# Kernel tuning notes

Hardware: AMD Instinct MI355X
Metric: run time of the kernel (lower is better)

The kernel has to match this reference:

```python
import jax, jax.numpy as jnp
import numpy as np

T, D, E, K, F, SF = 4096, 1024, 8, 2, 1024, 1024  # tokens, d_model, experts, top_k, moe_ff, shared_ff


def setup_inputs() -> dict:
    key = jax.random.key(0)
    ks = jax.random.split(key, 10)
    hidden_states = jax.random.normal(ks[0], (T, D), jnp.float32)
    # balanced expert assignment: the fused kernel's get_split_sizes assumes tokens
    # split evenly across experts after permute_tokens, so exactly T*K/E per expert
    flat = jnp.arange(T * K) % E
    flat = jax.random.permutation(ks[1], flat)
    topk_indices = flat.reshape(T, K).astype(jnp.int32)
    w = jax.random.uniform(ks[2], (T, K), jnp.float32)
    topk_weights = w / w.sum(-1, keepdims=True)  # norm_topk_prob
    s = 0.02
    w_gate = jax.random.normal(ks[3], (E, D, F), jnp.float32) * s
    w_up = jax.random.normal(ks[4], (E, D, F), jnp.float32) * s
    w_down = jax.random.normal(ks[5], (E, F, D), jnp.float32) * s
    sw_gate = jax.random.normal(ks[6], (D, SF), jnp.float32) * s
    sw_up = jax.random.normal(ks[7], (D, SF), jnp.float32) * s
    sw_down = jax.random.normal(ks[8], (SF, D), jnp.float32) * s
    shared_gate_w = jax.random.normal(ks[9], (D, 1), jnp.float32) * s
    return dict(hidden_states=hidden_states, topk_weights=topk_weights,
                w_gate=w_gate, w_up=w_up, w_down=w_down,
                sw_gate=sw_gate, sw_up=sw_up, sw_down=sw_down,
                shared_gate_w=shared_gate_w, topk_indices=topk_indices)


def _silu(x):
    return x * jax.nn.sigmoid(x)


def reference(hidden_states, topk_weights, w_gate, w_up, w_down,
              sw_gate, sw_up, sw_down, shared_gate_w, topk_indices):
    t, d = hidden_states.shape
    e = w_gate.shape[0]
    k = topk_indices.shape[1]
    c = (t * k) // e  # tokens per expert (balanced split, as in get_split_sizes)

    # permute_tokens: replicate each token top_k times and sort by expert id
    flat_idx = topk_indices.reshape(-1)                    # [t*k]
    order = jnp.argsort(flat_idx)                          # dispatch permutation
    x_rep = jnp.repeat(hidden_states, k, axis=0)           # [t*k, d]
    xs = x_rep[order].reshape(e, c, d)                     # grouped per-expert

    # per-expert gated MLP (grouped GEMMs)
    h = _silu(jnp.einsum('ecd,edf->ecf', xs, w_gate)) * jnp.einsum('ecd,edf->ecf', xs, w_up)
    y = jnp.einsum('ecf,efd->ecd', h, w_down).reshape(t * k, d)

    # unpermute_tokens + weighted combine over top_k
    y = y[jnp.argsort(order)].reshape(t, k, d)
    out = (y * topk_weights[..., None]).sum(axis=1)        # [t, d]

    # shared expert with sigmoid gate
    s = jnp.einsum('tf,fd->td', _silu(hidden_states @ sw_gate) * (hidden_states @ sw_up), sw_down)
    g = jax.nn.sigmoid(hidden_states @ shared_gate_w)      # [t, 1]
    return (out + g * s).astype(hidden_states.dtype)
```

## Files before the change

### kernel.cpp

```cpp
#include <hip/hip_runtime.h>
#include <hip/hip_bf16.h>
#include <cstdint>
#include <cstddef>

#define TTOK 4096
#define DM   1024
#define NE   8
#define KTOP 2
#define FFD  1024
#define CPER 1024
#define MROWS 12288


typedef __attribute__((ext_vector_type(8))) short frag8;
typedef __attribute__((ext_vector_type(4))) float f32x4;

static __device__ __forceinline__ unsigned short f2bf(float f) {
  unsigned int u = __float_as_uint(f);
  u += 0x7fff + ((u >> 16) & 1);
  return (unsigned short)(u >> 16);
}
static __device__ __forceinline__ float bf2f(unsigned short u) {
  return __uint_as_float((unsigned int)u << 16);
}

static __device__ __forceinline__ void gld_lds16(const unsigned short* g, unsigned short* l) {
  __builtin_amdgcn_global_load_lds(
      (const __attribute__((address_space(1))) unsigned int*)g,
      (__attribute__((address_space(3))) unsigned int*)l,
      16, 0, 0);
}

static __device__ __forceinline__ int lds_slot64(int r, int c) {
  return r * 8 + (c ^ (r & 7));
}

static __device__ __forceinline__ void stage_tile64(const unsigned short* __restrict__ src,
                                                    int row0, int k0,
                                                    unsigned short* lds, int tid) {
#pragma unroll
  for (int it = 0; it < 4; ++it) {
    int seg = it * 256 + tid;
    int r = seg >> 3;
    int cs = (seg & 7) ^ (r & 7);
    gld_lds16(src + (size_t)(row0 + r) * 1024 + k0 + cs * 8, lds + seg * 8);
  }
}

static __device__ __forceinline__ void swizzle_xy(int& x, int& y) {
  int L = blockIdx.y * 8 + blockIdx.x;
  int xcd = L & 7;
  int s = L >> 3;
  y = xcd * 12 + s % 12;
  x = s / 12;
}

static __device__ __forceinline__ void swizzle_xy4(int& x, int& y) {
  int L = blockIdx.y * 4 + blockIdx.x;
  int xcd = L & 7;
  int s = L >> 3;
  y = xcd * 12 + s % 12;
  x = s / 12;
}

__global__ void prep_transw_kernel(
    const float* __restrict__ wg, const float* __restrict__ wu,
    const float* __restrict__ wd, const float* __restrict__ sg,
    const float* __restrict__ su, const float* __restrict__ sd,
    unsigned short* __restrict__ owg, unsigned short* __restrict__ owu,
    unsigned short* __restrict__ owd,
    const float* __restrict__ x, const float* __restrict__ gw,
    const int* __restrict__ idx, const float* __restrict__ tw,
    int* __restrict__ cnt, int* __restrict__ rowsrc, int* __restrict__ inv,
    float* __restrict__ rowscale, unsigned short* __restrict__ xb) {
  int z = blockIdx.z;
  if (z == 27) {
    int bid = blockIdx.y * 4 + blockIdx.x;
    if (bid < 32) {
      int i = bid * 256 + threadIdx.x;
      int e = idx[i];
      int pos = atomicAdd(&cnt[e], 1);
      int j = e * CPER + pos;
      rowsrc[j] = i >> 1;
      rowscale[j] = tw[i];
      inv[i] = j;
      if (i < TTOK) rowsrc[8192 + i] = i;
    }
    int wave = threadIdx.x >> 6;
    int lane = threadIdx.x & 63;
    const float4* wr = (const float4*)gw;
#pragma unroll 2
    for (int s = 0; s < 16; ++s) {
      int row = bid * 64 + wave * 16 + s;
      const float4* xr = (const float4*)(x + (size_t)row * 1024);
      ushort4* ob = (ushort4*)(xb + (size_t)row * 1024);
      float acc = 0.f;
#pragma unroll
      for (int c = 0; c < 4; ++c) {
        int k = lane + 64 * c;
        float4 v = xr[k];
        float4 g = wr[k];
        acc += v.x * g.x + v.y * g.y + v.z * g.z + v.w * g.w;
        ushort4 o;
        o.x = f2bf(v.x); o.y = f2bf(v.y); o.z = f2bf(v.z); o.w = f2bf(v.w);
        ob[k] = o;
      }
#pragma unroll
      for (int off = 32; off; off >>= 1) acc += __shfl_down(acc, off);
      if (lane == 0) rowscale[8192 + row] = 1.f / (1.f + __expf(-acc));
    }
    return;
  }
  const float* src; unsigned short* dst;
  if (z < 8)       { src = wg + (size_t)z * 1048576;        dst = owg + (size_t)z * 1048576; }
  else if (z < 16) { src = wu + (size_t)(z - 8) * 1048576;  dst = owu + (size_t)(z - 8) * 1048576; }
  else if (z < 24) { src = wd + (size_t)(z - 16) * 1048576; dst = owd + (size_t)(z - 16) * 1048576; }
  else if (z == 24){ src = sg; dst = owg + (size_t)8 * 1048576; }
  else if (z == 25){ src = su; dst = owu + (size_t)8 * 1048576; }
  else             { src = sd; dst = owd + (size_t)8 * 1048576; }
  __shared__ float tile[64][65];
  int bx0 = blockIdx.x * 256;
  int by  = blockIdx.y * 64;
  int c4 = threadIdx.x & 15;
  int r0 = threadIdx.x >> 4;
  const float* sbase = src + (size_t)(by + r0) * 1024 + bx0 + c4 * 4;
  float4 v0 = *(const float4*)(sbase + 0);
  float4 v1 = *(const float4*)(sbase + 16384);
  float4 v2 = *(const float4*)(sbase + 32768);
  float4 v3 = *(const float4*)(sbase + 49152);
  float4 w0, w1, w2, w3;
#pragma unroll
  for (int t = 0; t < 4; ++t) {
    int bx = bx0 + t * 64;
    __syncthreads();
    tile[r0     ][c4 * 4 + 0] = v0.x; tile[r0     ][c4 * 4 + 1] = v0.y;
    tile[r0     ][c4 * 4 + 2] = v0.z; tile[r0     ][c4 * 4 + 3] = v0.w;
    tile[r0 + 16][c4 * 4 + 0] = v1.x; tile[r0 + 16][c4 * 4 + 1] = v1.y;
    tile[r0 + 16][c4 * 4 + 2] = v1.z; tile[r0 + 16][c4 * 4 + 3] = v1.w;
    tile[r0 + 32][c4 * 4 + 0] = v2.x; tile[r0 + 32][c4 * 4 + 1] = v2.y;
    tile[r0 + 32][c4 * 4 + 2] = v2.z; tile[r0 + 32][c4 * 4 + 3] = v2.w;
    tile[r0 + 48][c4 * 4 + 0] = v3.x; tile[r0 + 48][c4 * 4 + 1] = v3.y;
    tile[r0 + 48][c4 * 4 + 2] = v3.z; tile[r0 + 48][c4 * 4 + 3] = v3.w;
    if (t < 3) {
      const float* nb = sbase + (t + 1) * 64;
      w0 = *(const float4*)(nb + 0);
      w1 = *(const float4*)(nb + 16384);
      w2 = *(const float4*)(nb + 32768);
      w3 = *(const float4*)(nb + 49152);
    }
    __syncthreads();
#pragma unroll
    for (int i = 0; i < 4; ++i) {
      int f = r0 + 16 * i;
      ushort4 o;
      o.x = f2bf(tile[c4 * 4 + 0][f]);
      o.y = f2bf(tile[c4 * 4 + 1][f]);
      o.z = f2bf(tile[c4 * 4 + 2][f]);
      o.w = f2bf(tile[c4 * 4 + 3][f]);
      *(ushort4*)&dst[(size_t)(bx + f) * 1024 + by + c4 * 4] = o;
    }
    v0 = w0; v1 = w1; v2 = w2; v3 = w3;
  }
}

static __device__ __forceinline__ int eid_of(int y) { return (y < 64) ? (y >> 3) : 8; }

__global__ __launch_bounds__(256, 2) void gemm1_kernel(
    const unsigned short* __restrict__ A, const int* __restrict__ rowsrc,
    const unsigned short* __restrict__ Bg, const unsigned short* __restrict__ Bu,
    unsigned short* __restrict__ H) {
  __shared__ __align__(16) unsigned short As[128 * 64];
  __shared__ __align__(16) unsigned short Bgs[128 * 64];
  __shared__ __align__(16) unsigned short Bus[128 * 64];
  int tid = threadIdx.x;
  int bx, by;
  swizzle_xy(bx, by);
  int e = eid_of(by);
  int row0 = by * 128;
  int col0 = bx * 128;
  const unsigned short* Bge = Bg + (size_t)e * 1048576;
  const unsigned short* Bue = Bu + (size_t)e * 1048576;

  const unsigned short* pA[4];
#pragma unroll
  for (int it = 0; it < 4; ++it) {
    int seg = it * 256 + tid;
    int r = seg >> 3;
    int cs = (seg & 7) ^ (r & 7);
    pA[it] = A + (size_t)rowsrc[row0 + r] * 1024 + cs * 8;
  }

  int wave = tid >> 6, lane = tid & 63;
  int wm = wave >> 1, wn = wave & 1;
  int lr = lane & 15, q = lane >> 4;

  f32x4 accg[4][4], accu[4][4];
#pragma unroll
  for (int i = 0; i < 4; ++i)
#pragma unroll
    for (int j = 0; j < 4; ++j) {
      accg[i][j] = (f32x4){0.f, 0.f, 0.f, 0.f};
      accu[i][j] = (f32x4){0.f, 0.f, 0.f, 0.f};
    }

  for (int kt = 0; kt < 1024; kt += 64) {
#pragma unroll
    for (int it = 0; it < 4; ++it)
      gld_lds16(pA[it] + kt, As + (it * 256 + tid) * 8);
    stage_tile64(Bge, col0, kt, Bgs, tid);
    stage_tile64(Bue, col0, kt, Bus, tid);
    __syncthreads();
#pragma unroll
    for (int kk = 0; kk < 2; ++kk) {
      int c = kk * 4 + q;
      frag8 a[4], b0[4], b1[4];
#pragma unroll
      for (int i = 0; i < 4; ++i) {
        int r = wm * 64 + i * 16 + lr;
        a[i] = *(const frag8*)&As[lds_slot64(r, c) * 8];
      }
#pragma unroll
      for (int j = 0; j < 4; ++j) {
        int r = wn * 64 + j * 16 + lr;
        b0[j] = *(const frag8*)&Bgs[lds_slot64(r, c) * 8];
        b1[j] = *(const frag8*)&Bus[lds_slot64(r, c) * 8];
      }
#pragma unroll
      for (int i = 0; i < 4; ++i)
#pragma unroll
        for (int j = 0; j < 4; ++j) {
          accg[i][j] = __builtin_amdgcn_mfma_f32_16x16x32_bf16(a[i], b0[j], accg[i][j], 0, 0, 0);
          accu[i][j] = __builtin_amdgcn_mfma_f32_16x16x32_bf16(a[i], b1[j], accu[i][j], 0, 0, 0);
        }
    }
    __syncthreads();
  }
#pragma unroll
  for (int i = 0; i < 4; ++i)
#pragma unroll
    for (int j = 0; j < 4; ++j)
#pragma unroll
      for (int r = 0; r < 4; ++r) {
        int m = row0 + wm * 64 + i * 16 + q * 4 + r;
        int n = col0 + wn * 64 + j * 16 + lr;
        float gv = accg[i][j][r];
        float hv = gv / (1.f + __expf(-gv)) * accu[i][j][r];
        H[(size_t)m * 1024 + n] = f2bf(hv);
      }
}

__global__ __launch_bounds__(256, 2) void gemm2_kernel(
    const unsigned short* __restrict__ A, const unsigned short* __restrict__ B,
    const float* __restrict__ rowscale, unsigned short* __restrict__ Y) {
  __shared__ __align__(16) unsigned short As[128 * 64];
  __shared__ __align__(16) unsigned short Bs[256 * 64];
  int tid = threadIdx.x;
  int bx, by;
  swizzle_xy4(bx, by);
  int e = eid_of(by);
  int row0 = by * 128;
  int col0 = bx * 256;
  const unsigned short* Be = B + (size_t)e * 1048576;

  int wave = tid >> 6, lane = tid & 63;
  int wm = wave >> 1, wn = wave & 1;
  int lr = lane & 15, q = lane >> 4;

  f32x4 acc[4][8];
#pragma unroll
  for (int i = 0; i < 4; ++i)
#pragma unroll
    for (int j = 0; j < 8; ++j) acc[i][j] = (f32x4){0.f, 0.f, 0.f, 0.f};

  for (int kt = 0; kt < 1024; kt += 64) {
    stage_tile64(A, row0, kt, As, tid);
#pragma unroll
    for (int it = 0; it < 8; ++it) {
      int seg = it * 256 + tid;
      int r = seg >> 3;
      int cs = (seg & 7) ^ (r & 7);
      gld_lds16(Be + (size_t)(col0 + r) * 1024 + kt + cs * 8, Bs + seg * 8);
    }
    __syncthreads();
#pragma unroll
    for (int kk = 0; kk < 2; ++kk) {
      int c = kk * 4 + q;
      frag8 a[4], b[8];
#pragma unroll
      for (int i = 0; i < 4; ++i) {
        int r = wm * 64 + i * 16 + lr;
        a[i] = *(const frag8*)&As[lds_slot64(r, c) * 8];
      }
#pragma unroll
      for (int j = 0; j < 8; ++j) {
        int r = wn * 128 + j * 16 + lr;
        b[j] = *(const frag8*)&Bs[lds_slot64(r, c) * 8];
      }
#pragma unroll
      for (int i = 0; i < 4; ++i)
#pragma unroll
        for (int j = 0; j < 8; ++j)
          acc[i][j] = __builtin_amdgcn_mfma_f32_16x16x32_bf16(a[i], b[j], acc[i][j], 0, 0, 0);
    }
    __syncthreads();
  }
#pragma unroll
  for (int i = 0; i < 4; ++i)
#pragma unroll
    for (int r = 0; r < 4; ++r) {
      int m = row0 + wm * 64 + i * 16 + q * 4 + r;
      float sc = rowscale[m];
#pragma unroll
      for (int j = 0; j < 8; ++j) {
        int n = col0 + wn * 128 + j * 16 + lr;
        Y[(size_t)m * 1024 + n] = f2bf(sc * acc[i][j][r]);
      }
    }
}

__global__ void combine_kernel(const unsigned short* __restrict__ Y,
                               const int* __restrict__ inv, float* __restrict__ out) {
  int base = blockIdx.x * 256 + threadIdx.x;
#pragma unroll
  for (int k = 0; k < 2; ++k) {
    int slot = base + k * 524288;
    int t = slot >> 8;
    int c = slot & 255;
    int j0 = inv[2 * t], j1 = inv[2 * t + 1];
    ushort4 a = ((const ushort4*)(Y + (size_t)j0 * 1024))[c];
    ushort4 b = ((const ushort4*)(Y + (size_t)j1 * 1024))[c];
    ushort4 s = ((const ushort4*)(Y + (size_t)(8192 + t) * 1024))[c];
    float4 o;
    o.x = bf2f(a.x) + bf2f(b.x) + bf2f(s.x);
    o.y = bf2f(a.y) + bf2f(b.y) + bf2f(s.y);
    o.z = bf2f(a.z) + bf2f(b.z) + bf2f(s.z);
    o.w = bf2f(a.w) + bf2f(b.w) + bf2f(s.w);
    ((float4*)(out + (size_t)t * 1024))[c] = o;
  }
}

extern "C" void kernel_launch(void* const* d_in, const int* in_sizes, int n_in,
                              void* d_out, int out_size, void* d_ws, size_t ws_size,
                              hipStream_t stream) {
  (void)in_sizes; (void)n_in; (void)out_size; (void)ws_size;
  const float* hidden  = (const float*)d_in[0];
  const float* topk_w  = (const float*)d_in[1];
  const float* w_gate  = (const float*)d_in[2];
  const float* w_up    = (const float*)d_in[3];
  const float* w_down  = (const float*)d_in[4];
  const float* sw_gate = (const float*)d_in[5];
  const float* sw_up   = (const float*)d_in[6];
  const float* sw_down = (const float*)d_in[7];
  const float* sgw     = (const float*)d_in[8];
  const int*   topk_i  = (const int*)d_in[9];
  float* out = (float*)d_out;

  char* p = (char*)d_ws;
  auto alloc = [&](size_t bytes) {
    char* r = p;
    p += (bytes + 255) & ~(size_t)255;
    return r;
  };
  unsigned short* Wg_all = (unsigned short*)alloc((size_t)9 * 1048576 * 2);
  unsigned short* Wu_all = (unsigned short*)alloc((size_t)9 * 1048576 * 2);
  unsigned short* Wd_all = (unsigned short*)alloc((size_t)9 * 1048576 * 2);
  unsigned short* Xbf    = (unsigned short*)alloc((size_t)TTOK * 1024 * 2);
  unsigned short* Hall   = (unsigned short*)alloc((size_t)MROWS * 1024 * 2);
  unsigned short* Yall   = (unsigned short*)alloc((size_t)MROWS * 1024 * 2);
  int*   cnt      = (int*)alloc(NE * 4);
  int*   rowsrc   = (int*)alloc((size_t)MROWS * 4);
  int*   inv      = (int*)alloc((size_t)TTOK * KTOP * 4);
  float* rowscale = (float*)alloc((size_t)MROWS * 4);

  hipMemsetAsync(cnt, 0, NE * 4, stream);

  prep_transw_kernel<<<dim3(4, 16, 28), 256, 0, stream>>>(
      w_gate, w_up, w_down, sw_gate, sw_up, sw_down, Wg_all, Wu_all, Wd_all,
      hidden, sgw, topk_i, topk_w, cnt, rowsrc, inv, rowscale, Xbf);

  gemm1_kernel<<<dim3(8, 96), 256, 0, stream>>>(Xbf, rowsrc, Wg_all, Wu_all, Hall);
  gemm2_kernel<<<dim3(4, 96), 256, 0, stream>>>(Hall, Wd_all, rowscale, Yall);
  combine_kernel<<<2048, 256, 0, stream>>>(Yall, inv, out);
}
```

Baseline: 290.9 us.

## Restructure weight transpose into per-wave 32x32 tiles and spread routing prep across blocks

The weight transpose/convert kernel now has each wave transpose its own 32x32 tiles through a double-buffered per-wave LDS region, so the block-wide __syncthreads barriers go away. Each wave also prefetches the next tile while it writes the current one. The routing-table build and the hidden-state bf16 conversion plus gate-dot, which used to sit in one extra z-slice of blocks, are now folded into the first 512 blocks of the weight-conversion grid. This removes the serial tail slice and removes barrier stalls. The cost is some load imbalance, since those blocks do extra work, and narrower 64-byte write segments per row.

Measured after the change: 296.7 us. Within noise of the previous version (+2.0%).

```diff
diff --git a/kernel.cpp b/kernel.cpp
--- a/kernel.cpp
+++ b/kernel.cpp
@@ -73,25 +73,29 @@
     const int* __restrict__ idx, const float* __restrict__ tw,
     int* __restrict__ cnt, int* __restrict__ rowsrc, int* __restrict__ inv,
     float* __restrict__ rowscale, unsigned short* __restrict__ xb) {
+  __shared__ float tl[4][2][32 * 33];
+  int tid = threadIdx.x;
+  int lane = tid & 63, w = tid >> 6;
+  int bid = blockIdx.y * 8 + blockIdx.x;
   int z = blockIdx.z;
-  if (z == 27) {
-    int bid = blockIdx.y * 4 + blockIdx.x;
-    if (bid < 32) {
-      int i = bid * 256 + threadIdx.x;
-      int e = idx[i];
-      int pos = atomicAdd(&cnt[e], 1);
-      int j = e * CPER + pos;
-      rowsrc[j] = i >> 1;
-      rowscale[j] = tw[i];
-      inv[i] = j;
-      if (i < TTOK) rowsrc[8192 + i] = i;
-    }
-    int wave = threadIdx.x >> 6;
-    int lane = threadIdx.x & 63;
+  int B = z * 32 + bid;
+
+  if (B < 32) {
+    int i = B * 256 + tid;
+    int e = idx[i];
+    int pos = atomicAdd(&cnt[e], 1);
+    int j = e * CPER + pos;
+    rowsrc[j] = i >> 1;
+    rowscale[j] = tw[i];
+    inv[i] = j;
+    if (i < TTOK) rowsrc[8192 + i] = i;
+  }
+
+  if (B < 512) {
     const float4* wr = (const float4*)gw;
-#pragma unroll 2
-    for (int s = 0; s < 16; ++s) {
-      int row = bid * 64 + wave * 16 + s;
+#pragma unroll
+    for (int rr = 0; rr < 2; ++rr) {
+      int row = B * 8 + w * 2 + rr;
       const float4* xr = (const float4*)(x + (size_t)row * 1024);
       ushort4* ob = (ushort4*)(xb + (size_t)row * 1024);
       float acc = 0.f;
@@ -109,8 +113,8 @@
       for (int off = 32; off; off >>= 1) acc += __shfl_down(acc, off);
       if (lane == 0) rowscale[8192 + row] = 1.f / (1.f + __expf(-acc));
     }
-    return;
-  }
+  }
+
   const float* src; unsigned short* dst;
   if (z < 8)       { src = wg + (size_t)z * 1048576;        dst = owg + (size_t)z * 1048576; }
   else if (z < 16) { src = wu + (size_t)(z - 8) * 1048576;  dst = owu + (size_t)(z - 8) * 1048576; }
@@ -118,48 +122,58 @@
   else if (z == 24){ src = sg; dst = owg + (size_t)8 * 1048576; }
   else if (z == 25){ src = su; dst = owu + (size_t)8 * 1048576; }
   else             { src = sd; dst = owd + (size_t)8 * 1048576; }
-  __shared__ float tile[64][65];
-  int bx0 = blockIdx.x * 256;
-  int by  = blockIdx.y * 64;
-  int c4 = threadIdx.x & 15;
-  int r0 = threadIdx.x >> 4;
-  const float* sbase = src + (size_t)(by + r0) * 1024 + bx0 + c4 * 4;
-  float4 v0 = *(const float4*)(sbase + 0);
-  float4 v1 = *(const float4*)(sbase + 16384);
-  float4 v2 = *(const float4*)(sbase + 32768);
-  float4 v3 = *(const float4*)(sbase + 49152);
-  float4 w0, w1, w2, w3;
-#pragma unroll
-  for (int t = 0; t < 4; ++t) {
-    int bx = bx0 + t * 64;
-    __syncthreads();
-    tile[r0     ][c4 * 4 + 0] = v0.x; tile[r0     ][c4 * 4 + 1] = v0.y;
-    tile[r0     ][c4 * 4 + 2] = v0.z; tile[r0     ][c4 * 4 + 3] = v0.w;
-    tile[r0 + 16][c4 * 4 + 0] = v1.x; tile[r0 + 16][c4 * 4 + 1] = v1.y;
-    tile[r0 + 16][c4 * 4 + 2] = v1.z; tile[r0 + 16][c4 * 4 + 3] = v1.w;
-    tile[r0 + 32][c4 * 4 + 0] = v2.x; tile[r0 + 32][c4 * 4 + 1] = v2.y;
-    tile[r0 + 32][c4 * 4 + 2] = v2.z; tile[r0 + 32][c4 * 4 + 3] = v2.w;
-    tile[r0 + 48][c4 * 4 + 0] = v3.x; tile[r0 + 48][c4 * 4 + 1] = v3.y;
-    tile[r0 + 48][c4 * 4 + 2] = v3.z; tile[r0 + 48][c4 * 4 + 3] = v3.w;
-    if (t < 3) {
-      const float* nb = sbase + (t + 1) * 64;
-      w0 = *(const float4*)(nb + 0);
-      w1 = *(const float4*)(nb + 16384);
-      w2 = *(const float4*)(nb + 32768);
-      w3 = *(const float4*)(nb + 49152);
-    }
-    __syncthreads();
-#pragma unroll
-    for (int i = 0; i < 4; ++i) {
-      int f = r0 + 16 * i;
+
+  int W = bid * 4 + w;
+  float* L0 = &tl[w][0][0];
+  float* L1 = &tl[w][1][0];
+
+  int row_l = lane >> 3;
+  int ch_l  = lane & 7;
+  int j_l   = lane >> 3;
+  int kc_l  = lane & 7;
+
+  float4 cur[4];
+  {
+    int T = W;
+    const float* sb = src + (size_t)(T >> 5) * 32 * 1024 + (T & 31) * 32;
+#pragma unroll
+    for (int c = 0; c < 4; ++c)
+      cur[c] = *(const float4*)&sb[(size_t)(c * 8 + row_l) * 1024 + ch_l * 4];
+  }
+#pragma unroll
+  for (int s = 0; s < 8; ++s) {
+    float* L = (s & 1) ? L1 : L0;
+#pragma unroll
+    for (int c = 0; c < 4; ++c) {
+      int r = c * 8 + row_l;
+      L[r * 33 + ch_l * 4 + 0] = cur[c].x;
+      L[r * 33 + ch_l * 4 + 1] = cur[c].y;
+      L[r * 33 + ch_l * 4 + 2] = cur[c].z;
+      L[r * 33 + ch_l * 4 + 3] = cur[c].w;
+    }
+    float4 nxt[4];
+    if (s < 7) {
+      int T = (s + 1) * 128 + W;
+      const float* sb = src + (size_t)(T >> 5) * 32 * 1024 + (T & 31) * 32;
+#pragma unroll
+      for (int c = 0; c < 4; ++c)
+        nxt[c] = *(const float4*)&sb[(size_t)(c * 8 + row_l) * 1024 + ch_l * 4];
+    }
+    int T = s * 128 + W;
+    unsigned short* db = dst + (size_t)(T & 31) * 32 * 1024 + (T >> 5) * 32;
+#pragma unroll
+    for (int c = 0; c < 4; ++c) {
+      int j = c * 8 + j_l;
+      float f0 = L[(4 * kc_l + 0) * 33 + j];
+      float f1 = L[(4 * kc_l + 1) * 33 + j];
+      float f2 = L[(4 * kc_l + 2) * 33 + j];
+      float f3 = L[(4 * kc_l + 3) * 33 + j];
       ushort4 o;
-      o.x = f2bf(tile[c4 * 4 + 0][f]);
-      o.y = f2bf(tile[c4 * 4 + 1][f]);
-      o.z = f2bf(tile[c4 * 4 + 2][f]);
-      o.w = f2bf(tile[c4 * 4 + 3][f]);
-      *(ushort4*)&dst[(size_t)(bx + f) * 1024 + by + c4 * 4] = o;
-    }
-    v0 = w0; v1 = w1; v2 = w2; v3 = w3;
+      o.x = f2bf(f0); o.y = f2bf(f1); o.z = f2bf(f2); o.w = f2bf(f3);
+      *(ushort4*)&db[(size_t)j * 1024 + kc_l * 4] = o;
+    }
+#pragma unroll
+    for (int c = 0; c < 4; ++c) cur[c] = nxt[c];
   }
 }
 
@@ -374,7 +388,7 @@
 
   hipMemsetAsync(cnt, 0, NE * 4, stream);
 
-  prep_transw_kernel<<<dim3(4, 16, 28), 256, 0, stream>>>(
+  prep_transw_kernel<<<dim3(8, 4, 27), 256, 0, stream>>>(
       w_gate, w_up, w_down, sw_gate, sw_up, sw_down, Wg_all, Wu_all, Wd_all,
       hidden, sgw, topk_i, topk_w, cnt, rowsrc, inv, rowscale, Xbf);
 
```
